# Kernel optimization log

Measured on AMD Instinct MI355X. Metric: run time of the kernel, lower is better.

Reference implementation:

```python
import jax, jax.numpy as jnp
import numpy as np
from jax import lax

B, L, D = 4, 4096, 1024
H = 4
DK = D // H   # head_k_dim = 256
DV = D // H   # head_v_dim = 256
HID = max(8, D // 2)  # gate trunk hidden = 512
CHUNK = 32
CONV_K = 4
EPS = 1e-5


def silu(x):
    return x * jax.nn.sigmoid(x)


def l2norm(x):
    return x * lax.rsqrt(jnp.sum(x * x, -1, keepdims=True) + 1e-6)


def causal_dwconv_silu(x, w):
    # x: (b,l,d), w: (d,k). Depthwise causal conv1d followed by SiLU (ShortConvolution).
    k = w.shape[-1]
    xp = jnp.pad(x, ((0, 0), (k - 1, 0), (0, 0))).transpose(0, 2, 1)  # (b,d,l+k-1)
    y = lax.conv_general_dilated(xp, w[:, None, :], (1,), 'VALID',
                                 feature_group_count=w.shape[0])
    return silu(y.transpose(0, 2, 1))


def delta_rule_chunkwise(q, k, v, beta, chunk=CHUNK):
    # q,k: (b,h,l,dk), v: (b,h,l,dv), beta: (b,h,l). l assumed multiple of chunk.
    b, h, l, dk = q.shape
    dv = v.shape[-1]
    n = l // chunk
    q = l2norm(q)
    k = l2norm(k)
    v = v * beta[..., None]
    kb = k * beta[..., None]
    qc = q.reshape(b, h, n, chunk, dk)
    kc = k.reshape(b, h, n, chunk, dk)
    vc = v.reshape(b, h, n, chunk, dv)
    kbc = kb.reshape(b, h, n, chunk, dk)
    # In-chunk triangular inverse: the torch loop computes (I + tril(kb k^T, -1))^{-1}
    Lm = jnp.tril(kbc @ jnp.swapaxes(kc, -1, -2), -1)  # strictly lower
    eye = jnp.eye(chunk, dtype=q.dtype)
    Tinv = jax.scipy.linalg.solve_triangular(eye + Lm, jnp.broadcast_to(eye, Lm.shape), lower=True)
    u = Tinv @ vc   # (b,h,n,c,dv)
    w = Tinv @ kbc  # (b,h,n,c,dk)
    strict = jnp.triu(jnp.ones((chunk, chunk), bool), 1)

    def step(S, inp):
        q_i, k_i, u_i, w_i = inp  # (b,h,c,d)
        attn = jnp.where(strict, 0.0, q_i @ jnp.swapaxes(k_i, -1, -2))
        u_hat = u_i - w_i @ S
        o_i = q_i @ S + attn @ u_hat
        return S + jnp.swapaxes(k_i, -1, -2) @ u_hat, o_i

    S0 = jnp.zeros((b, h, dk, dv), q.dtype)
    xs = tuple(jnp.moveaxis(t, 2, 0) for t in (qc, kc, u, w))
    S, o = lax.scan(step, S0, xs)
    o = jnp.moveaxis(o, 0, 2).reshape(b, h, l, dv)
    return o, S


def ema_rule(v, gamma):
    # v: (b,h,l,d), gamma: (b,h,l). Causal EMA: s_t = g_t*s_{t-1} + (1-g_t)*v_t
    def step(state, inp):
        v_t, g_t = inp
        state = g_t[..., None] * state + (1.0 - g_t[..., None]) * v_t
        return state, state

    s0 = jnp.zeros((v.shape[0], v.shape[1], v.shape[3]), v.dtype)
    _, out = lax.scan(step, s0, (jnp.moveaxis(v, 2, 0), jnp.moveaxis(gamma, 2, 0)))
    return jnp.moveaxis(out, 0, 2)


def hierarchical_gate(x, Wtrunk, btrunk, Wcoarse, bcoarse, Wlocal, blocal, Wglobal, bglobal, log_temp_c, log_temp_f):
    b, l, _ = x.shape
    z = silu(x @ Wtrunk.T + btrunk)  # (b,l,HID)
    tc = (jax.nn.softplus(log_temp_c) + 1e-4)[None, None, :, None]  # (1,1,h,1)
    tf = (jax.nn.softplus(log_temp_f) + 1e-4)[None, None, :, None]
    pg = jax.nn.softmax((z @ Wcoarse.T + bcoarse).reshape(b, l, H, 2) / tc, axis=-1)
    q = jax.nn.softmax((z @ Wlocal.T + blocal).reshape(b, l, H, 2) / tf, axis=-1)
    r = jax.nn.softmax((z @ Wglobal.T + bglobal).reshape(b, l, H, 2) / tf, axis=-1)
    w_v = pg[..., 0:1] * q[..., 0:1]
    w_es = pg[..., 0:1] * q[..., 1:2]
    w_d = pg[..., 1:2] * r[..., 0:1]
    w_el = pg[..., 1:2] * r[..., 1:2]
    return jnp.concatenate([w_v, w_es, w_d, w_el], axis=-1)  # (b,l,h,4)


def setup_inputs() -> dict:
    key = jax.random.key(0)
    ks = jax.random.split(key, 20)
    s = 0.02
    inp = {
        'hidden_states': jax.random.normal(ks[0], (B, L, D), jnp.float32),
        'Wq': jax.random.normal(ks[1], (D, D), jnp.float32) * s,
        'Wk': jax.random.normal(ks[2], (D, D), jnp.float32) * s,
        'Wv': jax.random.normal(ks[3], (D, D), jnp.float32) * s,
        'conv_q_w': jax.random.normal(ks[4], (D, CONV_K), jnp.float32) * 0.5,
        'conv_k_w': jax.random.normal(ks[5], (D, CONV_K), jnp.float32) * 0.5,
        'conv_v_w': jax.random.normal(ks[6], (D, CONV_K), jnp.float32) * 0.5,
        'Wb': jax.random.normal(ks[7], (H, D), jnp.float32) * s,
        'Wds': jax.random.normal(ks[8], (H, D), jnp.float32) * s,
        'bds': jnp.full((H,), -2.9444, jnp.float32),
        'Wdl': jax.random.normal(ks[9], (H, D), jnp.float32) * s,
        'bdl': jnp.full((H,), 2.9444, jnp.float32),
        'Wtrunk': jax.random.normal(ks[10], (HID, D), jnp.float32) * s,
        'btrunk': jnp.zeros((HID,), jnp.float32),
        'Wcoarse': jax.random.normal(ks[11], (H * 2, HID), jnp.float32) * s,
        'bcoarse': jnp.ones((H * 2,), jnp.float32),
        'Wlocal': jax.random.normal(ks[12], (H * 2, HID), jnp.float32) * s,
        'blocal': jnp.zeros((H * 2,), jnp.float32).at[::2].set(1.0),
        'Wglobal': jax.random.normal(ks[13], (H * 2, HID), jnp.float32) * s,
        'bglobal': jnp.zeros((H * 2,), jnp.float32).at[::2].set(1.0),
        'log_temp_c': jnp.zeros((H,), jnp.float32),  # log(1.0)
        'log_temp_f': jnp.zeros((H,), jnp.float32),
        'o_norm_w': jnp.ones((DV,), jnp.float32),
        'Wo': jax.random.normal(ks[14], (D, D), jnp.float32) * s,
    }
    return inp


def reference(hidden_states, Wq, Wk, Wv, conv_q_w, conv_k_w, conv_v_w, Wb, Wds, bds, Wdl, bdl,
              Wtrunk, btrunk, Wcoarse, bcoarse, Wlocal, blocal, Wglobal, bglobal,
              log_temp_c, log_temp_f, o_norm_w, Wo):
    x = hidden_states
    b, l, _ = x.shape
    # projections + short causal depthwise conv + SiLU
    q = causal_dwconv_silu(x @ Wq.T, conv_q_w).reshape(b, l, H, DK).transpose(0, 2, 1, 3)
    k = causal_dwconv_silu(x @ Wk.T, conv_k_w).reshape(b, l, H, DK).transpose(0, 2, 1, 3)
    v = causal_dwconv_silu(x @ Wv.T, conv_v_w).reshape(b, l, H, DV).transpose(0, 2, 1, 3)
    beta = jax.nn.sigmoid(x @ Wb.T).transpose(0, 2, 1)  # (b,h,l)
    delta_o, _ = delta_rule_chunkwise(q, k, v, beta)
    g_s = jax.nn.sigmoid(x @ Wds.T + bds).transpose(0, 2, 1)  # (b,h,l) short decay
    g_l = jax.nn.sigmoid(x @ Wdl.T + bdl).transpose(0, 2, 1)  # long decay
    ema_s = ema_rule(v, g_s)
    ema_l = ema_rule(v, g_l)
    weights = hierarchical_gate(x, Wtrunk, btrunk, Wcoarse, bcoarse, Wlocal, blocal,
                                Wglobal, bglobal, log_temp_c, log_temp_f)  # (b,l,h,4) [V,Es,D,El]
    v_b = v.transpose(0, 2, 1, 3)
    o = (weights[..., 0:1] * v_b
         + weights[..., 1:2] * ema_s.transpose(0, 2, 1, 3)
         + weights[..., 2:3] * delta_o.transpose(0, 2, 1, 3)
         + weights[..., 3:4] * ema_l.transpose(0, 2, 1, 3))
    # per-head RMSNorm
    o = o * lax.rsqrt(jnp.mean(o * o, -1, keepdims=True) + EPS) * o_norm_w
    return o.reshape(b, l, D) @ Wo.T
```

## Files before the change

kernel.cpp:

```cpp
#include <hip/hip_runtime.h>
#include <math.h>

#define BB 4
#define LL 4096
#define DD 1024
#define HH 4
#define DKk 256
#define DVv 256
#define HIDD 512
#define NC 128
#define NSEG 64
#define SEG 64

typedef unsigned short ushort_t;
typedef __attribute__((ext_vector_type(8))) short short8;
typedef __attribute__((ext_vector_type(4))) float floatx4;

__device__ __forceinline__ float sigm(float x) { return 1.f / (1.f + __expf(-x)); }

__device__ __forceinline__ float bf2f(ushort_t u) {
  union { unsigned int i; float f; } c; c.i = ((unsigned int)u) << 16; return c.f;
}
__device__ __forceinline__ ushort_t f2bf(float f) {
  union { float f; unsigned int i; } c; c.f = f;
  unsigned int lsb = (c.i >> 16) & 1u;
  return (ushort_t)((c.i + 0x7fffu + lsb) >> 16);
}
__device__ __forceinline__ void unpack2(unsigned int u, float& a, float& b) {
  union { unsigned int i; float f; } c0, c1;
  c0.i = u << 16; c1.i = u & 0xffff0000u; a = c0.f; b = c1.f;
}
__device__ __forceinline__ unsigned int pack2(float a, float b) {
  return (unsigned int)f2bf(a) | ((unsigned int)f2bf(b) << 16);
}
__device__ __forceinline__ void unpack8(const uint4 v, float* o) {
  unpack2(v.x, o[0], o[1]); unpack2(v.y, o[2], o[3]);
  unpack2(v.z, o[4], o[5]); unpack2(v.w, o[6], o[7]);
}
__device__ __forceinline__ float ubits(unsigned u) {
  union { unsigned i; float f; } c; c.i = u; return c.f;
}
__device__ __forceinline__ void split2t(float a, float b, unsigned& hi, unsigned& lo) {
  union { float f; unsigned u; } ca, cb; ca.f = a; cb.f = b;
  const unsigned ha = ca.u & 0xffff0000u, hb = cb.u & 0xffff0000u;
  hi = (ha >> 16) | hb;
  union { float f; unsigned u; } la, lb;
  la.f = a - ubits(ha); lb.f = b - ubits(hb);
  lo = (la.u >> 16) | (lb.u & 0xffff0000u);
}
__device__ __forceinline__ void gload16(const ushort_t* g, ushort_t* l) {
  __builtin_amdgcn_global_load_lds(
      (const __attribute__((address_space(1))) void*)g,
      (__attribute__((address_space(3))) void*)l, 16, 0, 0);
}

__global__ __launch_bounds__(256) void cvt_all_kernel(
    const float* __restrict__ x,  const float* __restrict__ Wq,
    const float* __restrict__ Wk, const float* __restrict__ Wv,
    const float* __restrict__ Wo, const float* __restrict__ Wtr,
    ushort_t* __restrict__ xb,  ushort_t* __restrict__ Wqb,
    ushort_t* __restrict__ Wkb, ushort_t* __restrict__ Wvb,
    ushort_t* __restrict__ Wob, ushort_t* __restrict__ Wtrb)
{
  const int NX = (int)((size_t)BB*LL*DD/8), NW = DD*DD/8, NT = HIDD*DD/8;
  int i = blockIdx.x * 256 + threadIdx.x;
  const float* src; ushort_t* dst;
  if (i < NX) { src = x; dst = xb; }
  else {
    i -= NX;
    if (i < NW) { src = Wq; dst = Wqb; }
    else { i -= NW;
      if (i < NW) { src = Wk; dst = Wkb; }
      else { i -= NW;
        if (i < NW) { src = Wv; dst = Wvb; }
        else { i -= NW;
          if (i < NW) { src = Wo; dst = Wob; }
          else { i -= NW; if (i >= NT) return; src = Wtr; dst = Wtrb; }
        }
      }
    }
  }
  const float4 a = ((const float4*)src)[2*i];
  const float4 b = ((const float4*)src)[2*i + 1];
  uint4 p;
  p.x = pack2(a.x, a.y); p.y = pack2(a.z, a.w);
  p.z = pack2(b.x, b.y); p.w = pack2(b.z, b.w);
  ((uint4*)dst)[i] = p;
}

template<int ACT, int BF16OUT>
__global__ __launch_bounds__(256) void gemm_bf16(const ushort_t* __restrict__ A,
    const ushort_t* __restrict__ W, const float* __restrict__ bias,
    void* __restrict__ Cv, int M, int N, int K)
{
  __shared__ ushort_t As[128*32];
  __shared__ ushort_t Ws[128*32];
  const int tid = threadIdx.x;
  const int bm = blockIdx.y * 128, bn = blockIdx.x * 128;
  const int lane = tid & 63, wave = tid >> 6;
  const int wm = (wave >> 1) * 64, wn = (wave & 1) * 64;
  const int fr = lane & 15, fq = lane >> 4;
  const int srow = wave * 16 + (lane >> 2);
  const int scol = (lane & 3) * 8;
  const ushort_t* Ap = A + (size_t)(bm + srow) * K + scol;
  const ushort_t* Wp = W + (size_t)(bn + srow) * K + scol;
  ushort_t* AsD = &As[wave * 512];
  ushort_t* WsD = &Ws[wave * 512];
  floatx4 acc[4][4];
#pragma unroll
  for (int i = 0; i < 4; ++i)
#pragma unroll
    for (int j = 0; j < 4; ++j) acc[i][j] = (floatx4){0.f, 0.f, 0.f, 0.f};

  for (int k0 = 0; k0 < K; k0 += 32) {
    __syncthreads();
    gload16(Ap + k0, AsD);
    gload16(Ap + (size_t)64 * K + k0, AsD + 64*32);
    gload16(Wp + k0, WsD);
    gload16(Wp + (size_t)64 * K + k0, WsD + 64*32);
    __syncthreads();
    short8 af[4], bf_[4];
#pragma unroll
    for (int mt = 0; mt < 4; ++mt)
      af[mt] = *(const short8*)&As[(wm + mt*16 + fr)*32 + fq*8];
#pragma unroll
    for (int nt = 0; nt < 4; ++nt)
      bf_[nt] = *(const short8*)&Ws[(wn + nt*16 + fr)*32 + fq*8];
#pragma unroll
    for (int mt = 0; mt < 4; ++mt)
#pragma unroll
      for (int nt = 0; nt < 4; ++nt)
        acc[mt][nt] = __builtin_amdgcn_mfma_f32_16x16x32_bf16(af[mt], bf_[nt], acc[mt][nt], 0, 0, 0);
  }
#pragma unroll
  for (int mt = 0; mt < 4; ++mt) {
#pragma unroll
    for (int reg = 0; reg < 4; ++reg) {
      const int row = bm + wm + mt*16 + fq*4 + reg;
#pragma unroll
      for (int nt = 0; nt < 4; ++nt) {
        const int col = bn + wn + nt*16 + fr;
        float v = acc[mt][nt][reg];
        if (ACT == 1) { v += bias[col]; v = v * sigm(v); }
        if (BF16OUT) ((ushort_t*)Cv)[(size_t)row * N + col] = f2bf(v);
        else         ((float*)Cv)[(size_t)row * N + col] = v;
      }
    }
  }
}

__global__ __launch_bounds__(256) void conv_silu_kernel(const ushort_t* __restrict__ xin,
    const float* __restrict__ wc, ushort_t* __restrict__ outp)
{
  const size_t i8 = (size_t)blockIdx.x * 256 + threadIdx.x;
  const int d8 = (int)((i8 & 127) << 3);
  const int l  = (int)((i8 >> 7) & (LL - 1));
  const int b  = (int)(i8 >> 19);
  const ushort_t* xp = xin + i8 * 8;
  const uint4 z4 = (uint4){0u,0u,0u,0u};
  const uint4 v0 = *(const uint4*)xp;
  const uint4 v1 = (l >= 1) ? *(const uint4*)(xp - DD)   : z4;
  const uint4 v2 = (l >= 2) ? *(const uint4*)(xp - 2*DD) : z4;
  const uint4 v3 = (l >= 3) ? *(const uint4*)(xp - 3*DD) : z4;
  float x0[8], x1[8], x2[8], x3[8];
  unpack8(v0, x0); unpack8(v1, x1); unpack8(v2, x2); unpack8(v3, x3);
  unsigned pk[4];
#pragma unroll
  for (int p = 0; p < 4; ++p) {
    float o2[2];
#pragma unroll
    for (int q = 0; q < 2; ++q) {
      const int j = p*2 + q;
      const float4 w = *(const float4*)(wc + (d8 + j) * 4);
      float acc = w.w * x0[j];
      acc = fmaf(w.z, x1[j], acc);
      acc = fmaf(w.y, x2[j], acc);
      acc = fmaf(w.x, x3[j], acc);
      o2[q] = acc * sigm(acc);
    }
    pk[p] = pack2(o2[0], o2[1]);
  }
  const int h = d8 >> 8, dk = d8 & 255;
  *(uint4*)(outp + (((size_t)(b*HH + h))*LL + l)*DKk + dk) = *(uint4*)pk;
}

__global__ __launch_bounds__(256) void small_proj_kernel(const float* __restrict__ x,
   const float* __restrict__ Wb, const float* __restrict__ Wds, const float* __restrict__ bds,
   const float* __restrict__ Wdl, const float* __restrict__ bdl,
   float* __restrict__ beta, float* __restrict__ gs, float* __restrict__ gl)
{
  const int bl = blockIdx.x;
  const int t = threadIdx.x, wave = t >> 6, lane = t & 63;
  __shared__ float res[12];
  const float* xr = x + (size_t)bl * DD + lane * 16;
  const float4 x0 = *(const float4*)(xr);
  const float4 x1 = *(const float4*)(xr + 4);
  const float4 x2 = *(const float4*)(xr + 8);
  const float4 x3 = *(const float4*)(xr + 12);
  for (int rr = 0; rr < 3; ++rr) {
    const int r = wave * 3 + rr;
    const int mat = r >> 2, h = r & 3;
    const float* Wr = (mat == 0 ? Wb : (mat == 1 ? Wds : Wdl)) + (size_t)h * DD + lane * 16;
    const float4 w0 = *(const float4*)(Wr);
    const float4 w1 = *(const float4*)(Wr + 4);
    const float4 w2 = *(const float4*)(Wr + 8);
    const float4 w3 = *(const float4*)(Wr + 12);
    float p = x0.x*w0.x + x0.y*w0.y + x0.z*w0.z + x0.w*w0.w
            + x1.x*w1.x + x1.y*w1.y + x1.z*w1.z + x1.w*w1.w
            + x2.x*w2.x + x2.y*w2.y + x2.z*w2.z + x2.w*w2.w
            + x3.x*w3.x + x3.y*w3.y + x3.z*w3.z + x3.w*w3.w;
#pragma unroll
    for (int o = 1; o < 64; o <<= 1) p += __shfl_xor(p, o);
    if (lane == 0) res[r] = p;
  }
  __syncthreads();
  if (t < 12) {
    const int mat = t >> 2, h = t & 3;
    float v = res[t];
    if (mat == 1) v += bds[h];
    if (mat == 2) v += bdl[h];
    v = sigm(v);
    const int b = bl >> 12, l = bl & (LL - 1);
    const size_t o = ((size_t)(b*HH + h))*LL + l;
    (mat == 0 ? beta : (mat == 1 ? gs : gl))[o] = v;
  }
}

#define QS 264
__global__ __launch_bounds__(256) void prep_kernel(ushort_t* __restrict__ q,
    ushort_t* __restrict__ k, const ushort_t* __restrict__ v,
    const float* __restrict__ beta,
    ushort_t* __restrict__ u, ushort_t* __restrict__ w,
    ushort_t* __restrict__ ah, ushort_t* __restrict__ al)
{
  __shared__ ushort_t qb[32*QS];
  __shared__ ushort_t kb[32*QS];
  __shared__ float Lm[32*32];
  __shared__ float betas[32];
  const int bid = blockIdx.x;
  const int ci = bid & (NC - 1);
  const int bh = bid >> 7;
  const int t = threadIdx.x;
  const size_t base = ((size_t)bh * LL + ci*32) * DKk;
  if (t < 32) betas[t] = beta[(size_t)bh * LL + ci*32 + t];
  for (int i4 = t; i4 < 1024; i4 += 256) {
    const int r = i4 >> 5, e = (i4 & 31) * 8;
    *(uint4*)&qb[r*QS + e] = *(const uint4*)(q + base + r*256 + e);
    *(uint4*)&kb[r*QS + e] = *(const uint4*)(k + base + r*256 + e);
  }
  __syncthreads();
  {
    const int r = t >> 3, g = t & 7;
    const int e0 = g * 32;
    float qf[32], kf[32];
#pragma unroll
    for (int j = 0; j < 4; ++j) {
      const uint4 qv = *(const uint4*)&qb[r*QS + e0 + j*8];
      const uint4 kv = *(const uint4*)&kb[r*QS + e0 + j*8];
      unpack8(qv, qf + j*8); unpack8(kv, kf + j*8);
    }
    float sq = 0.f, sk = 0.f;
#pragma unroll
    for (int j = 0; j < 32; ++j) {
      sq = fmaf(qf[j], qf[j], sq);
      sk = fmaf(kf[j], kf[j], sk);
    }
#pragma unroll
    for (int o = 1; o < 8; o <<= 1) { sq += __shfl_xor(sq, o); sk += __shfl_xor(sk, o); }
    const float rq = rsqrtf(sq + 1e-6f), rk = rsqrtf(sk + 1e-6f);
#pragma unroll
    for (int j = 0; j < 4; ++j) {
      uint4 qo, ko;
      qo.x = pack2(qf[j*8+0]*rq, qf[j*8+1]*rq);
      qo.y = pack2(qf[j*8+2]*rq, qf[j*8+3]*rq);
      qo.z = pack2(qf[j*8+4]*rq, qf[j*8+5]*rq);
      qo.w = pack2(qf[j*8+6]*rq, qf[j*8+7]*rq);
      ko.x = pack2(kf[j*8+0]*rk, kf[j*8+1]*rk);
      ko.y = pack2(kf[j*8+2]*rk, kf[j*8+3]*rk);
      ko.z = pack2(kf[j*8+4]*rk, kf[j*8+5]*rk);
      ko.w = pack2(kf[j*8+6]*rk, kf[j*8+7]*rk);
      *(uint4*)&qb[r*QS + e0 + j*8] = qo;
      *(uint4*)&kb[r*QS + e0 + j*8] = ko;
    }
  }
  __syncthreads();
  for (int i4 = t; i4 < 1024; i4 += 256) {
    const int r = i4 >> 5, e = (i4 & 31) * 8;
    *(uint4*)(q + base + r*256 + e) = *(const uint4*)&qb[r*QS + e];
  }
  {
    unsigned int pk[16];
#pragma unroll
    for (int j = 0; j < 16; ++j)
      pk[j] = (unsigned int)kb[(2*j)*QS + t] | ((unsigned int)kb[(2*j+1)*QS + t] << 16);
    uint4* kd = (uint4*)(k + base + (size_t)t*32);
#pragma unroll
    for (int j = 0; j < 4; ++j) kd[j] = ((const uint4*)pk)[j];
  }
  {
    const int lane = t & 63, wv4 = t >> 6;
    const int fr = lane & 15, fq = lane >> 4;
    const int it = wv4 >> 1, jt = wv4 & 1;
    floatx4 dq = (floatx4){0.f,0.f,0.f,0.f};
    floatx4 dk2 = (floatx4){0.f,0.f,0.f,0.f};
#pragma unroll
    for (int ks = 0; ks < 8; ++ks) {
      const short8 bfk = *(const short8*)&kb[(jt*16+fr)*QS + ks*32 + fq*8];
      const short8 afq = *(const short8*)&qb[(it*16+fr)*QS + ks*32 + fq*8];
      const short8 afk = *(const short8*)&kb[(it*16+fr)*QS + ks*32 + fq*8];
      dq  = __builtin_amdgcn_mfma_f32_16x16x32_bf16(afq, bfk, dq, 0,0,0);
      dk2 = __builtin_amdgcn_mfma_f32_16x16x32_bf16(afk, bfk, dk2, 0,0,0);
    }
#pragma unroll
    for (int reg = 0; reg < 4; ++reg) {
      const int i = it*16 + fq*4 + reg;
      const int j = jt*16 + fr;
      const float av = (j <= i) ? dq[reg] : 0.f;
      const ushort_t hh = f2bf(av);
      const size_t aoff = ((size_t)bh*NC + ci)*1024 + (size_t)i*32 + j;
      ah[aoff] = hh;
      al[aoff] = f2bf(av - bf2f(hh));
      Lm[i*32 + j] = (j < i) ? betas[i] * dk2[reg] : 0.f;
    }
  }
  __syncthreads();
  {
    float cu[32], cw[32];
#pragma unroll
    for (int r = 0; r < 32; ++r) {
      cu[r] = bf2f(v[base + r*256 + t]) * betas[r];
      cw[r] = bf2f(kb[r*QS + t]) * betas[r];
    }
#pragma unroll
    for (int i = 1; i < 32; ++i) {
      float au = cu[i], aw = cw[i];
#pragma unroll
      for (int j = 0; j < i; ++j) {
        const float lm = Lm[i*32 + j];
        au = fmaf(-lm, cu[j], au);
        aw = fmaf(-lm, cw[j], aw);
      }
      cu[i] = au; cw[i] = aw;
    }
    {
      unsigned int pu[16];
#pragma unroll
      for (int j = 0; j < 16; ++j) pu[j] = pack2(cu[2*j], cu[2*j+1]);
      uint4* ud = (uint4*)(u + base + (size_t)t*32);
#pragma unroll
      for (int j = 0; j < 4; ++j) ud[j] = ((const uint4*)pu)[j];
    }
#pragma unroll
    for (int r = 0; r < 32; ++r) w[base + r*256 + t] = f2bf(cw[r]);
  }
}

#define S16(dv,kk) (((dv)<<8) + ((kk) ^ (((dv)&7)<<3)))
#define U16(dv,cr) (((dv)<<5) + ((cr) ^ (((dv)&3)<<3)))

__global__ __launch_bounds__(256, 1) void scan_gate_kernel(
    const ushort_t* __restrict__ qn, const ushort_t* __restrict__ kt,
    const ushort_t* __restrict__ ut, const ushort_t* __restrict__ w,
    const ushort_t* __restrict__ ah, const ushort_t* __restrict__ al,
    float* __restrict__ dout,
    const ushort_t* __restrict__ z,
    const float* __restrict__ Wc, const float* __restrict__ bc,
    const float* __restrict__ Wl, const float* __restrict__ bl_,
    const float* __restrict__ Wg, const float* __restrict__ bg,
    const float* __restrict__ ltc, const float* __restrict__ ltf,
    float* __restrict__ wgt)
{
  __shared__ ushort_t STh[16*256];
  __shared__ ushort_t STl[16*256];
  __shared__ ushort_t Uh[16*32];
  __shared__ ushort_t Ul[16*32];
  const int bid = blockIdx.x;
  const int t = threadIdx.x;

  if (bid >= 256) {
    const int bl = bid - 256;
    const int wave = t >> 6, lane = t & 63;
    float* res = (float*)STh;
    const uint4 zv = *(const uint4*)(z + (size_t)bl * HIDD + lane * 8);
    float zf[8]; unpack8(zv, zf);
    for (int rr = 0; rr < 6; ++rr) {
      const int r = wave * 6 + rr;
      const int mat = r >> 3, qi = r & 7;
      const float* Wr = (mat == 0 ? Wc : (mat == 1 ? Wl : Wg)) + (size_t)qi * HIDD + lane * 8;
      const float4 w0 = *(const float4*)(Wr);
      const float4 w1 = *(const float4*)(Wr + 4);
      float p = zf[0]*w0.x + zf[1]*w0.y + zf[2]*w0.z + zf[3]*w0.w
              + zf[4]*w1.x + zf[5]*w1.y + zf[6]*w1.z + zf[7]*w1.w;
#pragma unroll
      for (int o = 1; o < 64; o <<= 1) p += __shfl_xor(p, o);
      if (lane == 0) {
        const float* br = (mat == 0 ? bc : (mat == 1 ? bl_ : bg));
        res[r] = p + br[qi];
      }
    }
    __syncthreads();
    if (t < 4) {
      const float tc = logf(1.f + __expf(ltc[t])) + 1e-4f;
      const float tf = logf(1.f + __expf(ltf[t])) + 1e-4f;
      const float pg0 = sigm((res[2*t]     - res[2*t+1])     / tc);
      const float q0  = sigm((res[8+2*t]   - res[8+2*t+1])   / tf);
      const float r0  = sigm((res[16+2*t]  - res[16+2*t+1])  / tf);
      float* o = wgt + ((size_t)bl * HH + t) * 4;
      o[0] = pg0 * q0;         o[1] = pg0 * (1.f - q0);
      o[2] = (1.f - pg0) * r0; o[3] = (1.f - pg0) * (1.f - r0);
    }
    return;
  }

  const int bh = bid & 15, vs = bid >> 4;
  const int b = bh >> 2, h = bh & 3;
  const int lane = t & 63, wv = t >> 6;
  const int fr = lane & 15, fq = lane >> 4;
  const int mt = wv & 1;
  const bool isW = (wv < 2);

  for (int i = t; i < 512; i += 256) {
    ((uint4*)STh)[i] = (uint4){0u,0u,0u,0u};
    ((uint4*)STl)[i] = (uint4){0u,0u,0u,0u};
  }

  const size_t bhL = (size_t)bh * LL;
  const ushort_t* wqB = (isW ? w : qn) + bhL * DKk;
  const ushort_t* kB  = kt + bhL * DKk;
  const ushort_t* uB  = ut + bhL * DVv;
  const ushort_t* ahB = ah + (size_t)bh * NC * 1024;
  const ushort_t* alB = al + (size_t)bh * NC * 1024;
  float* oB = dout + (size_t)b * LL * DD + h * DVv + vs * 16 + fr;

  floatx4 Sacc[4];
#pragma unroll
  for (int i = 0; i < 4; ++i) Sacc[i] = (floatx4){0.f,0.f,0.f,0.f};

  short8 aw[8]; uint2 uu;
  auto loadA = [&](int ci) {
    const ushort_t* ap = wqB + (size_t)(ci*32 + mt*16 + fr) * DKk + fq*8;
#pragma unroll
    for (int ks = 0; ks < 8; ++ks) aw[ks] = *(const short8*)(ap + ks*32);
    if (isW)
      uu = *(const uint2*)(uB + (size_t)ci*8192 + (size_t)(vs*16 + fr)*32 + mt*16 + fq*4);
  };

  loadA(0);
  __syncthreads();

  for (int ci = 0; ci < NC; ++ci) {
    short8 kf[4];
    {
      const ushort_t* kp = kB + (size_t)ci*8192 + (size_t)(wv*64 + fr)*32 + fq*8;
#pragma unroll
      for (int m = 0; m < 4; ++m) kf[m] = *(const short8*)(kp + m*512);
    }
    short8 afh, afl;
    if (!isW) {
      afh = *(const short8*)(ahB + (size_t)ci*1024 + (mt*16+fr)*32 + fq*8);
      afl = *(const short8*)(alB + (size_t)ci*1024 + (mt*16+fr)*32 + fq*8);
    }
    floatx4 acc0, acc1;
    if (isW) {
      float u0,u1,u2,u3; unpack2(uu.x,u0,u1); unpack2(uu.y,u2,u3);
      acc0 = (floatx4){-u0,-u1,-u2,-u3};
      acc1 = (floatx4){0.f,0.f,0.f,0.f};
#pragma unroll
      for (int ks = 0; ks < 8; ++ks) {
        const short8 sh = *(const short8*)&STh[S16(fr, ks*32 + fq*8)];
        const short8 sl = *(const short8*)&STl[S16(fr, ks*32 + fq*8)];
        acc0 = __builtin_amdgcn_mfma_f32_16x16x32_bf16(aw[ks], sh, acc0, 0,0,0);
        acc1 = __builtin_amdgcn_mfma_f32_16x16x32_bf16(aw[ks], sl, acc1, 0,0,0);
      }
      const float v0 = -(acc0[0]+acc1[0]), v1 = -(acc0[1]+acc1[1]);
      const float v2 = -(acc0[2]+acc1[2]), v3 = -(acc0[3]+acc1[3]);
      unsigned ph0, pl0, ph1, pl1;
      split2t(v0, v1, ph0, pl0); split2t(v2, v3, ph1, pl1);
      *(uint2*)&Uh[U16(fr, mt*16 + fq*4)] = (uint2){ph0, ph1};
      *(uint2*)&Ul[U16(fr, mt*16 + fq*4)] = (uint2){pl0, pl1};
    } else {
      acc0 = (floatx4){0.f,0.f,0.f,0.f};
#pragma unroll
      for (int ks = 0; ks < 8; ++ks) {
        const short8 sh = *(const short8*)&STh[S16(fr, ks*32 + fq*8)];
        acc0 = __builtin_amdgcn_mfma_f32_16x16x32_bf16(aw[ks], sh, acc0, 0,0,0);
      }
    }
    __syncthreads();
    if (ci + 1 < NC) loadA(ci + 1);
    const short8 uhh = *(const short8*)&Uh[U16(fr, fq*8)];
    const short8 uhl = *(const short8*)&Ul[U16(fr, fq*8)];
    if (!isW) {
      acc0 = __builtin_amdgcn_mfma_f32_16x16x32_bf16(afh, uhh, acc0, 0,0,0);
      acc0 = __builtin_amdgcn_mfma_f32_16x16x32_bf16(afh, uhl, acc0, 0,0,0);
      acc0 = __builtin_amdgcn_mfma_f32_16x16x32_bf16(afl, uhh, acc0, 0,0,0);
      float* op = oB + (size_t)(ci*32 + mt*16 + fq*4) * DD;
#pragma unroll
      for (int r = 0; r < 4; ++r) op[(size_t)r * DD] = acc0[r];
    }
#pragma unroll
    for (int m = 0; m < 4; ++m) {
      Sacc[m] = __builtin_amdgcn_mfma_f32_16x16x32_bf16(kf[m], uhh, Sacc[m], 0,0,0);
      Sacc[m] = __builtin_amdgcn_mfma_f32_16x16x32_bf16(kf[m], uhl, Sacc[m], 0,0,0);
    }
#pragma unroll
    for (int m = 0; m < 4; ++m) {
      unsigned ph0, pl0, ph1, pl1;
      split2t(Sacc[m][0], Sacc[m][1], ph0, pl0);
      split2t(Sacc[m][2], Sacc[m][3], ph1, pl1);
      const int dk0 = wv*64 + m*16 + fq*4;
      *(uint2*)&STh[S16(fr, dk0)] = (uint2){ph0, ph1};
      *(uint2*)&STl[S16(fr, dk0)] = (uint2){pl0, pl1};
    }
    __syncthreads();
  }
}

__global__ __launch_bounds__(256) void ema_local_kernel(const ushort_t* __restrict__ v,
  const float* __restrict__ gs, const float* __restrict__ gl,
  ushort_t* __restrict__ es, ushort_t* __restrict__ el,
  float* __restrict__ Bs, float* __restrict__ Bl,
  float* __restrict__ As, float* __restrict__ Al,
  float* __restrict__ PfS, float* __restrict__ PfL)
{
  const int bid = blockIdx.x;
  const int seg = bid & (NSEG - 1), bh = bid >> 6;
  const int b = bh >> 2, h = bh & 3;
  const int dv = threadIdx.x;
  const int l0 = seg * SEG;
  const ushort_t* vp = v + ((size_t)bh*LL + l0) * DVv + dv;
  const float* gsp = gs + (size_t)bh*LL + l0;
  const float* glp = gl + (size_t)bh*LL + l0;
  ushort_t* esp = es + ((size_t)b*LL + l0)*DD + h*DVv + dv;
  ushort_t* elp = el + ((size_t)b*LL + l0)*DD + h*DVv + dv;
  float* pfs = PfS + (size_t)bh*LL + l0;
  float* pfl = PfL + (size_t)bh*LL + l0;
  float s1 = 0.f, s2 = 0.f, p1 = 1.f, p2 = 1.f;
  for (int j = 0; j < SEG; ++j) {
    const float vv = bf2f(vp[(size_t)j * DVv]);
    const float a = gsp[j], g2 = glp[j];
    s1 = fmaf(a,  s1, (1.f - a)  * vv);
    s2 = fmaf(g2, s2, (1.f - g2) * vv);
    p1 *= a; p2 *= g2;
    esp[(size_t)j * DD] = f2bf(s1);
    elp[(size_t)j * DD] = f2bf(s2);
    if (dv == 0) { pfs[j] = p1; pfl[j] = p2; }
  }
  const size_t o = (((size_t)bh*NSEG + seg) << 8) + dv;
  Bs[o] = s1; Bl[o] = s2;
  if (dv == 0) { As[bh*NSEG + seg] = p1; Al[bh*NSEG + seg] = p2; }
}

__global__ __launch_bounds__(256) void ema_carry_kernel(
  const float* __restrict__ Bs, const float* __restrict__ Bl,
  const float* __restrict__ As, const float* __restrict__ Al,
  float* __restrict__ Cs, float* __restrict__ Cl)
{
  const int bh = blockIdx.x;
  const int dv = threadIdx.x;
  __shared__ float Ash[NSEG], Alh[NSEG];
  if (dv < NSEG) { Ash[dv] = As[bh*NSEG + dv]; Alh[dv] = Al[bh*NSEG + dv]; }
  __syncthreads();
  float c1 = 0.f, c2 = 0.f;
  for (int s = 0; s < NSEG; ++s) {
    const size_t o = (((size_t)bh*NSEG + s) << 8) + dv;
    Cs[o] = c1; Cl[o] = c2;
    c1 = fmaf(Ash[s], c1, Bs[o]);
    c2 = fmaf(Alh[s], c2, Bl[o]);
  }
}

__global__ __launch_bounds__(64) void combine_kernel(const ushort_t* __restrict__ v,
  const ushort_t* __restrict__ es, const ushort_t* __restrict__ el,
  const float* __restrict__ dov, const float* __restrict__ wgt,
  const float* __restrict__ onw,
  const float* __restrict__ Cs, const float* __restrict__ Cl,
  const float* __restrict__ PfS, const float* __restrict__ PfL,
  ushort_t* __restrict__ outp)
{
  const int bid = blockIdx.x;
  const int h = bid & 3;
  const size_t bl = (size_t)(bid >> 2);
  const int lane = threadIdx.x;
  const size_t b = bl >> 12;
  const size_t l = bl & (LL - 1);
  const int bh = (int)(b * HH) + h;
  const int seg = (int)(l >> 6);
  const size_t vidx = (((b*HH + h) * (size_t)LL) + l) * DVv + lane*4;
  const size_t didx = bl * DD + h*DVv + lane*4;
  const uint2 vu = *(const uint2*)(v + vidx);
  const uint2 eu = *(const uint2*)(es + didx);
  const uint2 gu = *(const uint2*)(el + didx);
  const float4 d4 = *(const float4*)(dov + didx);
  const float pS = PfS[(size_t)bh*LL + l];
  const float pL = PfL[(size_t)bh*LL + l];
  const float4 cs4 = *(const float4*)(Cs + (((size_t)bh*NSEG + seg) << 8) + lane*4);
  const float4 cl4 = *(const float4*)(Cl + (((size_t)bh*NSEG + seg) << 8) + lane*4);
  float vf[4], ef[4], gf[4];
  unpack2(vu.x, vf[0], vf[1]); unpack2(vu.y, vf[2], vf[3]);
  unpack2(eu.x, ef[0], ef[1]); unpack2(eu.y, ef[2], ef[3]);
  unpack2(gu.x, gf[0], gf[1]); unpack2(gu.y, gf[2], gf[3]);
  ef[0] = fmaf(pS, cs4.x, ef[0]); ef[1] = fmaf(pS, cs4.y, ef[1]);
  ef[2] = fmaf(pS, cs4.z, ef[2]); ef[3] = fmaf(pS, cs4.w, ef[3]);
  gf[0] = fmaf(pL, cl4.x, gf[0]); gf[1] = fmaf(pL, cl4.y, gf[1]);
  gf[2] = fmaf(pL, cl4.z, gf[2]); gf[3] = fmaf(pL, cl4.w, gf[3]);
  const float* wp = wgt + (size_t)bid * 4;
  const float w0 = wp[0], w1 = wp[1], w2 = wp[2], w3 = wp[3];
  float o[4];
  const float df[4] = {d4.x, d4.y, d4.z, d4.w};
  float ss = 0.f;
#pragma unroll
  for (int i = 0; i < 4; ++i) {
    o[i] = w0*vf[i] + w1*ef[i] + w2*df[i] + w3*gf[i];
    ss = fmaf(o[i], o[i], ss);
  }
#pragma unroll
  for (int off = 1; off < 64; off <<= 1) ss += __shfl_xor(ss, off);
  const float sc = rsqrtf(ss * (1.f / DVv) + 1e-5f);
  const float4 nw = *(const float4*)(onw + lane*4);
  uint2 pk;
  pk.x = pack2(o[0]*sc*nw.x, o[1]*sc*nw.y);
  pk.y = pack2(o[2]*sc*nw.z, o[3]*sc*nw.w);
  *(uint2*)(outp + didx) = pk;
}

extern "C" void kernel_launch(void* const* d_in, const int* in_sizes, int n_in,
                              void* d_out, int out_size, void* d_ws, size_t ws_size,
                              hipStream_t stream)
{
  const float* x    = (const float*)d_in[0];
  const float* Wq   = (const float*)d_in[1];
  const float* Wk   = (const float*)d_in[2];
  const float* Wv   = (const float*)d_in[3];
  const float* cqw  = (const float*)d_in[4];
  const float* ckw  = (const float*)d_in[5];
  const float* cvw  = (const float*)d_in[6];
  const float* Wb   = (const float*)d_in[7];
  const float* Wds  = (const float*)d_in[8];
  const float* bds  = (const float*)d_in[9];
  const float* Wdl  = (const float*)d_in[10];
  const float* bdl  = (const float*)d_in[11];
  const float* Wtr  = (const float*)d_in[12];
  const float* btr  = (const float*)d_in[13];
  const float* Wc   = (const float*)d_in[14];
  const float* bc   = (const float*)d_in[15];
  const float* Wl   = (const float*)d_in[16];
  const float* blc  = (const float*)d_in[17];
  const float* Wg   = (const float*)d_in[18];
  const float* bg   = (const float*)d_in[19];
  const float* ltc  = (const float*)d_in[20];
  const float* ltf  = (const float*)d_in[21];
  const float* onw  = (const float*)d_in[22];
  const float* Wo   = (const float*)d_in[23];
  float* outp = (float*)d_out;

  const size_t BLD = (size_t)BB * LL * DD;
  unsigned char* w8 = (unsigned char*)d_ws;
  const size_t SL = BLD * 2;
  ushort_t* SA = (ushort_t*)(w8 + 0*SL);
  ushort_t* SB = (ushort_t*)(w8 + 1*SL);
  ushort_t* SC = (ushort_t*)(w8 + 2*SL);
  ushort_t* SD = (ushort_t*)(w8 + 3*SL);
  ushort_t* SE = (ushort_t*)(w8 + 4*SL);
  ushort_t* zb   = (ushort_t*)(w8 + 5*SL);
  ushort_t* attn_hi = (ushort_t*)(w8 + 5*SL + BLD);
  ushort_t* attn_lo = attn_hi + (size_t)BB*HH*NC*1024;
  float*    beta = (float*)(attn_hi + 2*(size_t)BB*HH*NC*1024);
  float*    gs   = beta + (size_t)BB*HH*LL;
  float*    gl   = gs   + (size_t)BB*HH*LL;
  float*    wgt  = gl   + (size_t)BB*HH*LL;
  float*    Bs   = wgt  + (size_t)BB*LL*HH*4;
  float*    Bl   = Bs   + (size_t)BB*HH*NSEG*256;
  float*    Cs   = Bl   + (size_t)BB*HH*NSEG*256;
  float*    Cl   = Cs   + (size_t)BB*HH*NSEG*256;
  float*    As   = Cl   + (size_t)BB*HH*NSEG*256;
  float*    Al   = As   + (size_t)BB*HH*NSEG;
  float*    PfS  = Al   + (size_t)BB*HH*NSEG;
  float*    PfL  = PfS  + (size_t)BB*HH*LL;
  ushort_t* Wqb  = (ushort_t*)(PfL + (size_t)BB*HH*LL);
  ushort_t* Wkb  = Wqb + (size_t)DD*DD;
  ushort_t* Wvb  = Wkb + (size_t)DD*DD;
  ushort_t* Wob  = Wvb + (size_t)DD*DD;
  ushort_t* Wtrb = Wob + (size_t)DD*DD;
  ushort_t* xb   = SD;
  float*    dov  = outp;

  const int MBL = BB * LL;
  dim3 blk256(256);

  {
    const int NTOT = (int)(BLD/8) + 4*(DD*DD/8) + HIDD*DD/8;
    cvt_all_kernel<<<dim3((NTOT + 255)/256), blk256, 0, stream>>>(
        x, Wq, Wk, Wv, Wo, Wtr, xb, Wqb, Wkb, Wvb, Wob, Wtrb);
  }

  gemm_bf16<0,1><<<dim3(DD/128, MBL/128), blk256, 0, stream>>>(xb, Wqb, nullptr, SA, MBL, DD, DD);
  gemm_bf16<0,1><<<dim3(DD/128, MBL/128), blk256, 0, stream>>>(xb, Wkb, nullptr, SB, MBL, DD, DD);
  gemm_bf16<0,1><<<dim3(DD/128, MBL/128), blk256, 0, stream>>>(xb, Wvb, nullptr, SC, MBL, DD, DD);
  gemm_bf16<1,1><<<dim3(HIDD/128, MBL/128), blk256, 0, stream>>>(xb, Wtrb, btr, zb, MBL, HIDD, DD);
  small_proj_kernel<<<dim3(MBL), blk256, 0, stream>>>(x, Wb, Wds, bds, Wdl, bdl, beta, gs, gl);
  conv_silu_kernel<<<dim3((unsigned)(BLD/8/256)), blk256, 0, stream>>>(SA, cqw, SD);
  conv_silu_kernel<<<dim3((unsigned)(BLD/8/256)), blk256, 0, stream>>>(SB, ckw, SA);
  conv_silu_kernel<<<dim3((unsigned)(BLD/8/256)), blk256, 0, stream>>>(SC, cvw, SB);
  prep_kernel<<<dim3(BB*HH*NC), blk256, 0, stream>>>(SD, SA, SB, beta, SC, SE, attn_hi, attn_lo);
  scan_gate_kernel<<<dim3(256 + MBL), blk256, 0, stream>>>(
      SD, SA, SC, SE, attn_hi, attn_lo, dov,
      zb, Wc, bc, Wl, blc, Wg, bg, ltc, ltf, wgt);
  ema_local_kernel<<<dim3(BB*HH*NSEG), blk256, 0, stream>>>(SB, gs, gl, SE, SD, Bs, Bl, As, Al, PfS, PfL);
  ema_carry_kernel<<<dim3(BB*HH), blk256, 0, stream>>>(Bs, Bl, As, Al, Cs, Cl);
  combine_kernel<<<dim3(MBL*HH), dim3(64), 0, stream>>>(SB, SE, SD, dov, wgt, onw, Cs, Cl, PfS, PfL, SA);
  gemm_bf16<0,0><<<dim3(DD/128, MBL/128), blk256, 0, stream>>>(SA, Wob, nullptr, outp, MBL, DD, DD);
}
```

Baseline: 1.046 ms.

## Split gate work out of scan kernel and double-buffer scan fragment loads

The gate projection, which was previously co-launched as extra blocks of the scan kernel, now runs as its own kernel before the scan. The scan loop is unrolled by two with ping-pong register buffers, so the K, attention and A fragments for the next chunk are issued at the start of the current chunk rather than after the first barrier. This hides global-load latency in the serial chunk recurrence. The cost is higher register pressure, a separate gate launch, and losing any overlap the gate blocks had with the scan.

```diff
diff --git a/kernel.cpp b/kernel.cpp
--- a/kernel.cpp
+++ b/kernel.cpp
@@ -226,6 +226,46 @@
   }
 }
 
+__global__ __launch_bounds__(256) void gate_kernel(const ushort_t* __restrict__ z,
+  const float* __restrict__ Wc, const float* __restrict__ bc,
+  const float* __restrict__ Wl, const float* __restrict__ bl_,
+  const float* __restrict__ Wg, const float* __restrict__ bg,
+  const float* __restrict__ ltc, const float* __restrict__ ltf,
+  float* __restrict__ wgt)
+{
+  const int bl = blockIdx.x;
+  const int t = threadIdx.x, wave = t >> 6, lane = t & 63;
+  __shared__ float res[24];
+  const uint4 zv = *(const uint4*)(z + (size_t)bl * HIDD + lane * 8);
+  float zf[8]; unpack8(zv, zf);
+  for (int rr = 0; rr < 6; ++rr) {
+    const int r = wave * 6 + rr;
+    const int mat = r >> 3, qi = r & 7;
+    const float* Wr = (mat == 0 ? Wc : (mat == 1 ? Wl : Wg)) + (size_t)qi * HIDD + lane * 8;
+    const float4 w0 = *(const float4*)(Wr);
+    const float4 w1 = *(const float4*)(Wr + 4);
+    float p = zf[0]*w0.x + zf[1]*w0.y + zf[2]*w0.z + zf[3]*w0.w
+            + zf[4]*w1.x + zf[5]*w1.y + zf[6]*w1.z + zf[7]*w1.w;
+#pragma unroll
+    for (int o = 1; o < 64; o <<= 1) p += __shfl_xor(p, o);
+    if (lane == 0) {
+      const float* br = (mat == 0 ? bc : (mat == 1 ? bl_ : bg));
+      res[r] = p + br[qi];
+    }
+  }
+  __syncthreads();
+  if (t < 4) {
+    const float tc = logf(1.f + __expf(ltc[t])) + 1e-4f;
+    const float tf = logf(1.f + __expf(ltf[t])) + 1e-4f;
+    const float pg0 = sigm((res[2*t]     - res[2*t+1])     / tc);
+    const float q0  = sigm((res[8+2*t]   - res[8+2*t+1])   / tf);
+    const float r0  = sigm((res[16+2*t]  - res[16+2*t+1])  / tf);
+    float* o = wgt + ((size_t)bl * HH + t) * 4;
+    o[0] = pg0 * q0;         o[1] = pg0 * (1.f - q0);
+    o[2] = (1.f - pg0) * r0; o[3] = (1.f - pg0) * (1.f - r0);
+  }
+}
+
 #define QS 264
 __global__ __launch_bounds__(256) void prep_kernel(ushort_t* __restrict__ q,
     ushort_t* __restrict__ k, const ushort_t* __restrict__ v,
@@ -358,63 +398,23 @@
 #define S16(dv,kk) (((dv)<<8) + ((kk) ^ (((dv)&7)<<3)))
 #define U16(dv,cr) (((dv)<<5) + ((cr) ^ (((dv)&3)<<3)))
 
-__global__ __launch_bounds__(256, 1) void scan_gate_kernel(
+struct FragsK { short8 kf[4]; short8 afh, afl; };
+struct FragsA { short8 aw[8]; uint2 uu; };
+
+__global__ __launch_bounds__(256, 1) void scan_kernel(
     const ushort_t* __restrict__ qn, const ushort_t* __restrict__ kt,
     const ushort_t* __restrict__ ut, const ushort_t* __restrict__ w,
     const ushort_t* __restrict__ ah, const ushort_t* __restrict__ al,
-    float* __restrict__ dout,
-    const ushort_t* __restrict__ z,
-    const float* __restrict__ Wc, const float* __restrict__ bc,
-    const float* __restrict__ Wl, const float* __restrict__ bl_,
-    const float* __restrict__ Wg, const float* __restrict__ bg,
-    const float* __restrict__ ltc, const float* __restrict__ ltf,
-    float* __restrict__ wgt)
+    float* __restrict__ dout)
 {
   __shared__ ushort_t STh[16*256];
   __shared__ ushort_t STl[16*256];
   __shared__ ushort_t Uh[16*32];
   __shared__ ushort_t Ul[16*32];
   const int bid = blockIdx.x;
-  const int t = threadIdx.x;
-
-  if (bid >= 256) {
-    const int bl = bid - 256;
-    const int wave = t >> 6, lane = t & 63;
-    float* res = (float*)STh;
-    const uint4 zv = *(const uint4*)(z + (size_t)bl * HIDD + lane * 8);
-    float zf[8]; unpack8(zv, zf);
-    for (int rr = 0; rr < 6; ++rr) {
-      const int r = wave * 6 + rr;
-      const int mat = r >> 3, qi = r & 7;
-      const float* Wr = (mat == 0 ? Wc : (mat == 1 ? Wl : Wg)) + (size_t)qi * HIDD + lane * 8;
-      const float4 w0 = *(const float4*)(Wr);
-      const float4 w1 = *(const float4*)(Wr + 4);
-      float p = zf[0]*w0.x + zf[1]*w0.y + zf[2]*w0.z + zf[3]*w0.w
-              + zf[4]*w1.x + zf[5]*w1.y + zf[6]*w1.z + zf[7]*w1.w;
-#pragma unroll
-      for (int o = 1; o < 64; o <<= 1) p += __shfl_xor(p, o);
-      if (lane == 0) {
-        const float* br = (mat == 0 ? bc : (mat == 1 ? bl_ : bg));
-        res[r] = p + br[qi];
-      }
-    }
-    __syncthreads();
-    if (t < 4) {
-      const float tc = logf(1.f + __expf(ltc[t])) + 1e-4f;
-      const float tf = logf(1.f + __expf(ltf[t])) + 1e-4f;
-      const float pg0 = sigm((res[2*t]     - res[2*t+1])     / tc);
-      const float q0  = sigm((res[8+2*t]   - res[8+2*t+1])   / tf);
-      const float r0  = sigm((res[16+2*t]  - res[16+2*t+1])  / tf);
-      float* o = wgt + ((size_t)bl * HH + t) * 4;
-      o[0] = pg0 * q0;         o[1] = pg0 * (1.f - q0);
-      o[2] = (1.f - pg0) * r0; o[3] = (1.f - pg0) * (1.f - r0);
-    }
-    return;
-  }
-
   const int bh = bid & 15, vs = bid >> 4;
   const int b = bh >> 2, h = bh & 3;
-  const int lane = t & 63, wv = t >> 6;
+  const int t = threadIdx.x, lane = t & 63, wv = t >> 6;
   const int fr = lane & 15, fq = lane >> 4;
   const int mt = wv & 1;
   const bool isW = (wv < 2);
@@ -436,41 +436,41 @@
 #pragma unroll
   for (int i = 0; i < 4; ++i) Sacc[i] = (floatx4){0.f,0.f,0.f,0.f};
 
-  short8 aw[8]; uint2 uu;
-  auto loadA = [&](int ci) {
+  auto loadK = [&](int ci, FragsK& f) {
+    const ushort_t* kp = kB + (size_t)ci*8192 + (size_t)(wv*64 + fr)*32 + fq*8;
+#pragma unroll
+    for (int m = 0; m < 4; ++m) f.kf[m] = *(const short8*)(kp + m*512);
+    if (!isW) {
+      f.afh = *(const short8*)(ahB + (size_t)ci*1024 + (mt*16+fr)*32 + fq*8);
+      f.afl = *(const short8*)(alB + (size_t)ci*1024 + (mt*16+fr)*32 + fq*8);
+    }
+  };
+  auto loadA = [&](int ci, FragsA& f) {
     const ushort_t* ap = wqB + (size_t)(ci*32 + mt*16 + fr) * DKk + fq*8;
 #pragma unroll
-    for (int ks = 0; ks < 8; ++ks) aw[ks] = *(const short8*)(ap + ks*32);
+    for (int ks = 0; ks < 8; ++ks) f.aw[ks] = *(const short8*)(ap + ks*32);
     if (isW)
-      uu = *(const uint2*)(uB + (size_t)ci*8192 + (size_t)(vs*16 + fr)*32 + mt*16 + fq*4);
+      f.uu = *(const uint2*)(uB + (size_t)ci*8192 + (size_t)(vs*16 + fr)*32 + mt*16 + fq*4);
   };
 
-  loadA(0);
+  FragsK k0, k1; FragsA a0, a1;
+  loadK(0, k0);
+  loadA(0, a0);
   __syncthreads();
 
-  for (int ci = 0; ci < NC; ++ci) {
-    short8 kf[4];
-    {
-      const ushort_t* kp = kB + (size_t)ci*8192 + (size_t)(wv*64 + fr)*32 + fq*8;
-#pragma unroll
-      for (int m = 0; m < 4; ++m) kf[m] = *(const short8*)(kp + m*512);
-    }
-    short8 afh, afl;
-    if (!isW) {
-      afh = *(const short8*)(ahB + (size_t)ci*1024 + (mt*16+fr)*32 + fq*8);
-      afl = *(const short8*)(alB + (size_t)ci*1024 + (mt*16+fr)*32 + fq*8);
-    }
+  auto body = [&](int ci, FragsK& kc, FragsK& kn, FragsA& ac, FragsA& an) {
+    if (ci + 1 < NC) { loadK(ci + 1, kn); loadA(ci + 1, an); }
     floatx4 acc0, acc1;
     if (isW) {
-      float u0,u1,u2,u3; unpack2(uu.x,u0,u1); unpack2(uu.y,u2,u3);
+      float u0,u1,u2,u3; unpack2(ac.uu.x,u0,u1); unpack2(ac.uu.y,u2,u3);
       acc0 = (floatx4){-u0,-u1,-u2,-u3};
       acc1 = (floatx4){0.f,0.f,0.f,0.f};
 #pragma unroll
       for (int ks = 0; ks < 8; ++ks) {
         const short8 sh = *(const short8*)&STh[S16(fr, ks*32 + fq*8)];
         const short8 sl = *(const short8*)&STl[S16(fr, ks*32 + fq*8)];
-        acc0 = __builtin_amdgcn_mfma_f32_16x16x32_bf16(aw[ks], sh, acc0, 0,0,0);
-        acc1 = __builtin_amdgcn_mfma_f32_16x16x32_bf16(aw[ks], sl, acc1, 0,0,0);
+        acc0 = __builtin_amdgcn_mfma_f32_16x16x32_bf16(ac.aw[ks], sh, acc0, 0,0,0);
+        acc1 = __builtin_amdgcn_mfma_f32_16x16x32_bf16(ac.aw[ks], sl, acc1, 0,0,0);
       }
       const float v0 = -(acc0[0]+acc1[0]), v1 = -(acc0[1]+acc1[1]);
       const float v2 = -(acc0[2]+acc1[2]), v3 = -(acc0[3]+acc1[3]);
@@ -483,25 +483,24 @@
 #pragma unroll
       for (int ks = 0; ks < 8; ++ks) {
         const short8 sh = *(const short8*)&STh[S16(fr, ks*32 + fq*8)];
-        acc0 = __builtin_amdgcn_mfma_f32_16x16x32_bf16(aw[ks], sh, acc0, 0,0,0);
+        acc0 = __builtin_amdgcn_mfma_f32_16x16x32_bf16(ac.aw[ks], sh, acc0, 0,0,0);
       }
     }
     __syncthreads();
-    if (ci + 1 < NC) loadA(ci + 1);
     const short8 uhh = *(const short8*)&Uh[U16(fr, fq*8)];
     const short8 uhl = *(const short8*)&Ul[U16(fr, fq*8)];
     if (!isW) {
-      acc0 = __builtin_amdgcn_mfma_f32_16x16x32_bf16(afh, uhh, acc0, 0,0,0);
-      acc0 = __builtin_amdgcn_mfma_f32_16x16x32_bf16(afh, uhl, acc0, 0,0,0);
-      acc0 = __builtin_amdgcn_mfma_f32_16x16x32_bf16(afl, uhh, acc0, 0,0,0);
+      acc0 = __builtin_amdgcn_mfma_f32_16x16x32_bf16(kc.afh, uhh, acc0, 0,0,0);
+      acc0 = __builtin_amdgcn_mfma_f32_16x16x32_bf16(kc.afh, uhl, acc0, 0,0,0);
+      acc0 = __builtin_amdgcn_mfma_f32_16x16x32_bf16(kc.afl, uhh, acc0, 0,0,0);
       float* op = oB + (size_t)(ci*32 + mt*16 + fq*4) * DD;
 #pragma unroll
       for (int r = 0; r < 4; ++r) op[(size_t)r * DD] = acc0[r];
     }
 #pragma unroll
     for (int m = 0; m < 4; ++m) {
-      Sacc[m] = __builtin_amdgcn_mfma_f32_16x16x32_bf16(kf[m], uhh, Sacc[m], 0,0,0);
-      Sacc[m] = __builtin_amdgcn_mfma_f32_16x16x32_bf16(kf[m], uhl, Sacc[m], 0,0,0);
+      Sacc[m] = __builtin_amdgcn_mfma_f32_16x16x32_bf16(kc.kf[m], uhh, Sacc[m], 0,0,0);
+      Sacc[m] = __builtin_amdgcn_mfma_f32_16x16x32_bf16(kc.kf[m], uhl, Sacc[m], 0,0,0);
     }
 #pragma unroll
     for (int m = 0; m < 4; ++m) {
@@ -513,6 +512,11 @@
       *(uint2*)&STl[S16(fr, dk0)] = (uint2){pl0, pl1};
     }
     __syncthreads();
+  };
+
+  for (int c2 = 0; c2 < NC; c2 += 2) {
+    body(c2,     k0, k1, a0, a1);
+    body(c2 + 1, k1, k0, a1, a0);
   }
 }
 
@@ -699,13 +703,12 @@
   gemm_bf16<0,1><<<dim3(DD/128, MBL/128), blk256, 0, stream>>>(xb, Wvb, nullptr, SC, MBL, DD, DD);
   gemm_bf16<1,1><<<dim3(HIDD/128, MBL/128), blk256, 0, stream>>>(xb, Wtrb, btr, zb, MBL, HIDD, DD);
   small_proj_kernel<<<dim3(MBL), blk256, 0, stream>>>(x, Wb, Wds, bds, Wdl, bdl, beta, gs, gl);
+  gate_kernel<<<dim3(MBL), blk256, 0, stream>>>(zb, Wc, bc, Wl, blc, Wg, bg, ltc, ltf, wgt);
   conv_silu_kernel<<<dim3((unsigned)(BLD/8/256)), blk256, 0, stream>>>(SA, cqw, SD);
   conv_silu_kernel<<<dim3((unsigned)(BLD/8/256)), blk256, 0, stream>>>(SB, ckw, SA);
   conv_silu_kernel<<<dim3((unsigned)(BLD/8/256)), blk256, 0, stream>>>(SC, cvw, SB);
   prep_kernel<<<dim3(BB*HH*NC), blk256, 0, stream>>>(SD, SA, SB, beta, SC, SE, attn_hi, attn_lo);
-  scan_gate_kernel<<<dim3(256 + MBL), blk256, 0, stream>>>(
-      SD, SA, SC, SE, attn_hi, attn_lo, dov,
-      zb, Wc, bc, Wl, blc, Wg, bg, ltc, ltf, wgt);
+  scan_kernel<<<dim3(256), blk256, 0, stream>>>(SD, SA, SC, SE, attn_hi, attn_lo, dov);
   ema_local_kernel<<<dim3(BB*HH*NSEG), blk256, 0, stream>>>(SB, gs, gl, SE, SD, Bs, Bl, As, Al, PfS, PfL);
   ema_carry_kernel<<<dim3(BB*HH), blk256, 0, stream>>>(Bs, Bl, As, Al, Cs, Cl);
   combine_kernel<<<dim3(MBL*HH), dim3(64), 0, stream>>>(SB, SE, SD, dov, wgt, onw, Cs, Cl, PfS, PfL, SA);
```

Measured after the change: 1.034 ms. About the same (-1.2%).
